# Optimization experiments

Measured on AMD Instinct MI355X. Metric: run time of the kernel, lower is better.

The kernel has to match this reference:

```python
import jax, jax.numpy as jnp
import numpy as np
import math

DIM = 1024
MAX_DEPTH = 16
ROPE_BASE = 10000.0
NUM_ACTIVE = 2

def setup_inputs() -> dict:
    key = jax.random.key(0)
    ks = jax.random.split(key, 6)
    bsz, seq, dim, E, hidden = 4, 1024, DIM, 8, 4 * DIM
    bound = 1.0 / math.sqrt(dim)
    return {
        "x": jax.random.normal(ks[0], (bsz, seq, dim), jnp.float32),
        "router_w": jax.random.normal(ks[1], (dim, dim), jnp.float32) * 0.02,
        "expert_keys": jax.random.uniform(ks[2], (E, dim), jnp.float32, -bound, bound),
        "expert_bias": jnp.zeros((E,), jnp.float32),
        "fc_w": jax.random.normal(ks[3], (E, hidden, dim), jnp.float32) * 0.02,
        "proj_w": jax.random.normal(ks[4], (E, dim, hidden), jnp.float32) * 0.02,
        "depth_idx": 3,
    }

def _rope_row(depth_idx, rev_idx, dtype):
    half = DIM // 2
    inv_freq = 1.0 / (ROPE_BASE ** (jnp.arange(0, DIM, 2, dtype=jnp.float32) / DIM))  # [half]
    f = depth_idx * inv_freq
    r = rev_idx * inv_freq
    return (jnp.cos(f).astype(dtype), jnp.sin(f).astype(dtype),
            jnp.cos(r).astype(dtype), jnp.sin(r).astype(dtype))

def reference(x, router_w, expert_keys, expert_bias, fc_w, proj_w, depth_idx):
    bsz, seq, dim = x.shape
    N = bsz * seq
    flat_x = x.reshape(N, dim)
    # router + RMSNorm (no weight, eps = machine eps, matching F.rms_norm default)
    q = flat_x @ router_w.T
    eps = jnp.asarray(jnp.finfo(q.dtype).eps, q.dtype)
    q = q * jax.lax.rsqrt(jnp.mean(q * q, axis=-1, keepdims=True) + eps)
    # depth RoPE (forward freq on first half pairing, reverse freq on second half)
    half = dim // 2
    cos, sin, rcos, rsin = _rope_row(float(depth_idx), float(MAX_DEPTH - 1 - depth_idx), q.dtype)
    q1, q2 = q[..., :half], q[..., half:]
    q = jnp.concatenate((q1 * cos + q2 * sin, -q1 * rsin + q2 * rcos), axis=-1)
    # routing
    logits = (q @ expert_keys.T) / math.sqrt(dim)  # [N, E]
    gate_values = jax.nn.sigmoid(logits)
    biased = logits + expert_bias
    _, topk_idx = jax.lax.top_k(biased, NUM_ACTIVE)  # [N, k]
    topk_gates = jnp.take_along_axis(gate_values, topk_idx, axis=-1)
    topk_gates = topk_gates / jnp.clip(topk_gates.sum(-1, keepdims=True), 1e-9, None)
    gates = jnp.zeros_like(gate_values).at[jnp.arange(N)[:, None], topk_idx].set(topk_gates)
    # dense all-expert MLP: relu(x W_fc^T)^2 W_proj^T, then mask-and-sum
    h = jax.nn.relu(jnp.einsum('nd,ehd->neh', flat_x, fc_w))
    expert_out = jnp.einsum('neh,edh->ned', h * h, proj_w)  # [N, E, dim]
    y = jnp.einsum('ned,ne->nd', expert_out, gates)
    return y.reshape(bsz, seq, dim)
```

## Files before the change

### kernel.cpp

```cpp
#include <hip/hip_runtime.h>
#include <hip/hip_bf16.h>
#include <math.h>

#define N_TOK 4096
#define DIM_V 1024
#define NEXP  8
#define HID   4096
#define NSLOT 9216

typedef short  s16x8 __attribute__((ext_vector_type(8)));
typedef unsigned short u16x8 __attribute__((ext_vector_type(8)));
typedef float  f32x4 __attribute__((ext_vector_type(4)));

constexpr size_t OFF_XB   = 0;
constexpr size_t OFF_WB   = OFF_XB + 8388608;
constexpr size_t OFF_RK   = OFF_WB + 2097152;
constexpr size_t OFF_KPP  = OFF_RK + 65536;
constexpr size_t OFF_SSQ  = OFF_KPP + 65536;
constexpr size_t OFF_CNT  = OFF_SSQ + 16384;
constexpr size_t OFF_CUR  = OFF_CNT + 128;
constexpr size_t OFF_TOK  = OFF_CUR + 128;
constexpr size_t OFF_GSL  = OFF_TOK + 36864;
constexpr size_t ZERO_BEG = OFF_KPP;
constexpr size_t ZERO_END = OFF_GSL + 36864;
constexpr size_t OFF_OFFP = ZERO_END;
constexpr size_t OFF_IDX2 = OFF_OFFP + 128;
constexpr size_t OFF_G2   = OFF_IDX2 + 32768;
constexpr size_t OFF_INV  = OFF_G2 + 32768;
constexpr size_t SMALL_END = OFF_INV + 32768;

constexpr size_t A_OFF_FCB = SMALL_END;
constexpr size_t A_OFF_PO  = A_OFF_FCB;
constexpr size_t A_OFF_PJB = A_OFF_FCB + 67108864;
constexpr size_t A_OFF_H2  = A_OFF_PJB + 67108864;
constexpr size_t WS_FULL   = A_OFF_H2 + 75497472;

__device__ inline unsigned short f2bf(float f) {
  __hip_bfloat16 h = __float2bfloat16(f);
  return __builtin_bit_cast(unsigned short, h);
}

__device__ __forceinline__ void gload16(const void* g, void* l) {
  __builtin_amdgcn_global_load_lds(
      (const __attribute__((address_space(1))) unsigned int*)g,
      (__attribute__((address_space(3))) unsigned int*)l, 16, 0, 0);
}

__global__ __launch_bounds__(256) void k_cvt_all(
    const float* __restrict__ x, const float* __restrict__ rw,
    const float* __restrict__ fw, const float* __restrict__ pw,
    unsigned short* __restrict__ xb, unsigned short* __restrict__ wb,
    unsigned short* __restrict__ fcb, unsigned short* __restrict__ pjb) {
  constexpr int NX = (N_TOK * DIM_V) / 4;
  constexpr int NW = (DIM_V * DIM_V) / 4;
  constexpr int NF = (NEXP * HID * DIM_V) / 4;
  const int cb[5] = {0, NX, NX + NW, NX + NW + NF, NX + NW + 2 * NF};
  const float* sp[4] = {x, rw, fw, pw};
  unsigned short* dp[4] = {xb, wb, fcb, pjb};
  const int total = cb[4];
  const int per = (total + (int)gridDim.x - 1) / (int)gridDim.x;
  const int beg = (int)blockIdx.x * per;
  const int end = (beg + per < total) ? beg + per : total;
#pragma unroll
  for (int r = 0; r < 4; ++r) {
    int rb = beg > cb[r] ? beg : cb[r];
    int re = end < cb[r + 1] ? end : cb[r + 1];
    const float4* s = (const float4*)sp[r];
    unsigned short* d = dp[r];
    for (int i = rb + (int)threadIdx.x; i < re; i += 256) {
      int j = i - cb[r];
      float4 v = s[j];
      ushort4 o = { f2bf(v.x), f2bf(v.y), f2bf(v.z), f2bf(v.w) };
      *(ushort4*)(d + (size_t)j * 4) = o;
    }
  }
}

__global__ void k_ropekeys(const float* __restrict__ keys, const int* __restrict__ depth,
                           double* __restrict__ rk) {
  int i = threadIdx.x;
  if (i >= 512) return;
  int dep = depth[0];
  double p = pow(10000.0, (double)i / 512.0);
  float invf = 1.0f / (float)p;
  float ff = (float)dep * invf;
  float rr = (float)(15 - dep) * invf;
  float cf  = (float)cos((double)ff);
  float sf  = (float)sin((double)ff);
  float rcf = (float)cos((double)rr);
  float rsf = (float)sin((double)rr);
  for (int e = 0; e < NEXP; ++e) {
    double k1 = (double)keys[e * DIM_V + i];
    double k2 = (double)keys[e * DIM_V + 512 + i];
    rk[e * DIM_V + i]       = (double)cf  * k1 - (double)rsf * k2;
    rk[e * DIM_V + 512 + i] = (double)sf  * k1 + (double)rcf * k2;
  }
}

__global__ __launch_bounds__(256) void k_colsum(const float* __restrict__ W,
                                                const double* __restrict__ rk,
                                                double* __restrict__ kpp) {
  int j  = blockIdx.x * 256 + threadIdx.x;
  int d0 = blockIdx.y * 64;
  double acc[NEXP] = {};
  for (int dd = 0; dd < 64; ++dd) {
    int d = d0 + dd;
    double w = (double)W[(size_t)d * DIM_V + j];
#pragma unroll
    for (int e = 0; e < NEXP; ++e) acc[e] += w * rk[e * DIM_V + d];
  }
  for (int e = 0; e < NEXP; ++e) atomicAdd(&kpp[e * DIM_V + j], acc[e]);
}

__global__ __launch_bounds__(256) void k_gate(const float* __restrict__ x,
                                              const double* __restrict__ kpp,
                                              const float* __restrict__ sumsq,
                                              const float* __restrict__ bias,
                                              int* __restrict__ idx2, float* __restrict__ gates2,
                                              int* __restrict__ counts) {
  int wave = (blockIdx.x * 256 + threadIdx.x) >> 6;
  int lane = threadIdx.x & 63;
  if (wave >= N_TOK) return;
  const float4* xr = (const float4*)(x + (size_t)wave * DIM_V);
  double a[NEXP] = {};
#pragma unroll
  for (int j = 0; j < 4; ++j) {
    int c = lane + 64 * j;
    float4 v = xr[c];
#pragma unroll
    for (int e = 0; e < NEXP; ++e) {
      const double* kp = kpp + (size_t)e * DIM_V + c * 4;
      a[e] += (double)v.x * kp[0] + (double)v.y * kp[1] +
              (double)v.z * kp[2] + (double)v.w * kp[3];
    }
  }
#pragma unroll
  for (int e = 0; e < NEXP; ++e)
    for (int d = 1; d < 64; d <<= 1) a[e] += __shfl_xor(a[e], d, 64);
  if (lane == 0) {
    float s = rsqrtf(sumsq[wave] * (1.0f / 1024.0f) + 1.1920928955078125e-7f);
    float z[NEXP], b[NEXP];
#pragma unroll
    for (int e = 0; e < NEXP; ++e) {
      z[e] = (float)(a[e] * (double)s * (1.0 / 32.0));
      b[e] = z[e] + bias[e];
    }
    int i1 = 0;
    for (int e = 1; e < NEXP; ++e) if (b[e] > b[i1]) i1 = e;
    int i2 = -1;
    for (int e = 0; e < NEXP; ++e) if (e != i1 && (i2 < 0 || b[e] > b[i2])) i2 = e;
    float g1 = 1.f / (1.f + expf(-z[i1]));
    float g2 = 1.f / (1.f + expf(-z[i2]));
    float sm = fmaxf(g1 + g2, 1e-9f);
    idx2[wave * 2] = i1; idx2[wave * 2 + 1] = i2;
    gates2[wave * 2] = g1 / sm; gates2[wave * 2 + 1] = g2 / sm;
    atomicAdd(&counts[i1], 1); atomicAdd(&counts[i2], 1);
  }
}

__global__ void k_scatter(const int* __restrict__ idx2, const float* __restrict__ gates2,
                          const int* __restrict__ counts, int* __restrict__ cursor,
                          int* __restrict__ tok, float* __restrict__ gsl,
                          int* __restrict__ inv, int* __restrict__ offp_out) {
  int off[NEXP + 1];
  off[0] = 0;
  for (int e = 0; e < NEXP; ++e) off[e + 1] = off[e] + ((counts[e] + 127) & ~127);
  int n = blockIdx.x * 256 + threadIdx.x;
  if (blockIdx.x == 0 && threadIdx.x == 0)
    for (int e = 0; e <= NEXP; ++e) offp_out[e] = off[e];
  if (n >= N_TOK) return;
  for (int r = 0; r < 2; ++r) {
    int e = idx2[n * 2 + r];
    int pos = atomicAdd(&cursor[e], 1);
    int slot = off[e] + pos;
    tok[slot] = n; gsl[slot] = gates2[n * 2 + r]; inv[n * 2 + r] = slot;
  }
}

__global__ __launch_bounds__(512) void k_fc256(
    const unsigned short* __restrict__ xb,
    const unsigned short* __restrict__ fcb,
    const int* __restrict__ offp, const int* __restrict__ tok,
    unsigned short* __restrict__ h2) {
  constexpr int KD = DIM_V;
  constexpr int NT = KD / 64;
  const int G = gridDim.x, q = G >> 3;
  const int idp = ((int)blockIdx.x & 7) * q + ((int)blockIdx.x >> 3);
  const int bx = idp >> 4;
  const int n0 = (idp & 15) * 256;
  int c = 0, e = 0, m0 = -1;
  for (e = 0; e < NEXP; ++e) {
    int nb = (offp[e + 1] - offp[e] + 255) >> 8;
    if (bx < c + nb) { m0 = offp[e] + (bx - c) * 256; break; }
    c += nb;
  }
  if (m0 < 0) return;
  const int segend = offp[e + 1];
  const unsigned short* Bp = fcb + ((size_t)e * HID + n0) * KD;

  __shared__ alignas(16) char smem[131072];
  const int tid = threadIdx.x, wid = tid >> 6, lane = tid & 63;
  const int wr = (wid >> 2) * 128, wcc = (wid & 3) * 64;
  const int swc8 = ((tid & 7) ^ ((tid >> 3) & 7)) * 8;
  const int frow = lane & 15, fsl = lane >> 4, fkey = lane & 7;

  int arow[4];
#pragma unroll
  for (int p = 0; p < 4; ++p) {
    int rr = m0 + p * 64 + (tid >> 3);
    arow[p] = tok[rr < NSLOT ? rr : NSLOT - 1];
  }

  auto stage = [&](int k0s, unsigned db) {
#pragma unroll
    for (int p = 0; p < 4; ++p)
      gload16(xb + (size_t)arow[p] * KD + k0s + swc8,
              smem + db + p * 8192 + wid * 1024);
#pragma unroll
    for (int p = 0; p < 4; ++p)
      gload16(Bp + (size_t)(p * 64 + (tid >> 3)) * KD + k0s + swc8,
              smem + db + 32768 + p * 8192 + wid * 1024);
  };

  f32x4 acc[8][4] = {};
  stage(0, 0);
  for (int t = 0; t < NT; ++t) {
    int tn = t + 1; if (tn == NT) tn = 0;
    stage(tn * 64, (unsigned)((t + 1) & 1) * 65536u);
    asm volatile("s_waitcnt vmcnt(8)" ::: "memory");
    __builtin_amdgcn_s_barrier();
    __builtin_amdgcn_sched_barrier(0);
    const unsigned Ab = (unsigned)(t & 1) * 65536u, Bb = Ab + 32768u;
#pragma unroll
    for (int kk2 = 0; kk2 < 2; ++kk2) {
      const unsigned so = (unsigned)(((fsl + kk2 * 4) ^ fkey) << 4);
      s16x8 af[8], bfr[4];
#pragma unroll
      for (int m = 0; m < 8; ++m)
        af[m] = *(const s16x8*)(smem + Ab + (unsigned)(wr + m * 16 + frow) * 128 + so);
#pragma unroll
      for (int n = 0; n < 4; ++n)
        bfr[n] = *(const s16x8*)(smem + Bb + (unsigned)(wcc + n * 16 + frow) * 128 + so);
      __builtin_amdgcn_s_setprio(1);
#pragma unroll
      for (int m = 0; m < 8; ++m)
#pragma unroll
        for (int n = 0; n < 4; ++n)
          acc[m][n] = __builtin_amdgcn_mfma_f32_16x16x32_bf16(af[m], bfr[n], acc[m][n], 0, 0, 0);
      __builtin_amdgcn_s_setprio(0);
    }
    __builtin_amdgcn_sched_barrier(0);
    __builtin_amdgcn_s_barrier();
  }
#pragma unroll
  for (int m = 0; m < 8; ++m)
#pragma unroll
    for (int j = 0; j < 4; ++j) {
      const int grow = m0 + wr + m * 16 + (lane >> 4) * 4 + j;
      if (grow < segend) {
#pragma unroll
        for (int n = 0; n < 4; ++n) {
          float v = acc[m][n][j];
          v = v > 0.f ? v * v : 0.f;
          h2[(size_t)grow * HID + n0 + wcc + n * 16 + (lane & 15)] = f2bf(v);
        }
      }
    }
}

__global__ __launch_bounds__(512) void k_proj256(
    const unsigned short* __restrict__ h2,
    const unsigned short* __restrict__ pjb,
    const int* __restrict__ offp, const float* __restrict__ gsl,
    float* __restrict__ po) {
  constexpr int KD = HID;
  constexpr int NT = KD / 64;
  const int G = gridDim.x, q = G >> 3;
  const int idp = ((int)blockIdx.x & 7) * q + ((int)blockIdx.x >> 3);
  const int bx = idp >> 4;
  const int n0 = (idp & 15) * 64;
  int c = 0, e = 0, m0 = -1;
  for (e = 0; e < NEXP; ++e) {
    int nb = (offp[e + 1] - offp[e] + 255) >> 8;
    if (bx < c + nb) { m0 = offp[e] + (bx - c) * 256; break; }
    c += nb;
  }
  if (m0 < 0) return;
  const int segend = offp[e + 1];
  const unsigned short* Bp = pjb + ((size_t)e * DIM_V + n0) * KD;

  __shared__ alignas(16) char smem[81920];
  const int tid = threadIdx.x, wid = tid >> 6, lane = tid & 63;
  const int wr = (wid >> 1) * 64, wc = (wid & 1) * 32;
  const int swc8 = ((tid & 7) ^ ((tid >> 3) & 7)) * 8;
  const int frow = lane & 15, fsl = lane >> 4, fkey = lane & 7;

  int arow[4];
#pragma unroll
  for (int p = 0; p < 4; ++p) {
    int rr = m0 + p * 64 + (tid >> 3);
    arow[p] = rr < NSLOT ? rr : NSLOT - 1;
  }

  auto stage = [&](int k0s, unsigned db) {
#pragma unroll
    for (int p = 0; p < 4; ++p)
      gload16(h2 + (size_t)arow[p] * KD + k0s + swc8,
              smem + db + p * 8192 + wid * 1024);
    gload16(Bp + (size_t)(tid >> 3) * KD + k0s + swc8,
            smem + db + 32768 + wid * 1024);
  };

  f32x4 acc[4][2] = {};
  stage(0, 0);
  for (int t = 0; t < NT; ++t) {
    int tn = t + 1; if (tn == NT) tn = 0;
    stage(tn * 64, (unsigned)((t + 1) & 1) * 40960u);
    asm volatile("s_waitcnt vmcnt(5)" ::: "memory");
    __builtin_amdgcn_s_barrier();
    __builtin_amdgcn_sched_barrier(0);
    const unsigned Ab = (unsigned)(t & 1) * 40960u, Bb = Ab + 32768u;
#pragma unroll
    for (int kk2 = 0; kk2 < 2; ++kk2) {
      const unsigned so = (unsigned)(((fsl + kk2 * 4) ^ fkey) << 4);
      s16x8 af[4], bfr[2];
#pragma unroll
      for (int m = 0; m < 4; ++m)
        af[m] = *(const s16x8*)(smem + Ab + (unsigned)(wr + m * 16 + frow) * 128 + so);
#pragma unroll
      for (int n = 0; n < 2; ++n)
        bfr[n] = *(const s16x8*)(smem + Bb + (unsigned)(wc + n * 16 + frow) * 128 + so);
      __builtin_amdgcn_s_setprio(1);
#pragma unroll
      for (int m = 0; m < 4; ++m)
#pragma unroll
        for (int n = 0; n < 2; ++n)
          acc[m][n] = __builtin_amdgcn_mfma_f32_16x16x32_bf16(af[m], bfr[n], acc[m][n], 0, 0, 0);
      __builtin_amdgcn_s_setprio(0);
    }
    __builtin_amdgcn_sched_barrier(0);
    __builtin_amdgcn_s_barrier();
  }
#pragma unroll
  for (int m = 0; m < 4; ++m)
#pragma unroll
    for (int j = 0; j < 4; ++j) {
      const int grow = m0 + wr + m * 16 + (lane >> 4) * 4 + j;
      if (grow < segend) {
        const float g = gsl[grow];
#pragma unroll
        for (int n = 0; n < 2; ++n)
          po[(size_t)grow * DIM_V + n0 + wc + n * 16 + (lane & 15)] = acc[m][n][j] * g;
      }
    }
}

__global__ __launch_bounds__(256) void k_qt(
    const unsigned short* __restrict__ Aptr,
    const unsigned short* __restrict__ Wptr,
    float* __restrict__ sumsq) {
  constexpr int KD = DIM_V;
  constexpr int GNB = DIM_V / 128;
  constexpr int NT  = KD / 64;
  const int G = gridDim.x, q = G >> 3;
  const int idp = ((int)blockIdx.x & 7) * q + ((int)blockIdx.x >> 3);
  const int n0 = (idp % GNB) * 128, m0 = (idp / GNB) * 128;
  const unsigned short* Bp = Wptr + (size_t)n0 * KD;

  __shared__ alignas(16) char smem[65536];
  const int tid = threadIdx.x, wid = tid >> 6, lane = tid & 63;
  const int wr = (wid >> 1) * 64, wc = (wid & 1) * 64;
  const int rql  = tid >> 3;
  const int swc8 = ((tid & 7) ^ ((tid >> 3) & 7)) * 8;
  const int frow = lane & 15, fsl = lane >> 4, fkey = lane & 7;

  auto stage = [&](int k0s, unsigned db) {
#pragma unroll
    for (int p = 0; p < 4; ++p)
      gload16(Aptr + (size_t)(m0 + p * 32 + rql) * KD + k0s + swc8,
              smem + db + p * 4096 + wid * 1024);
#pragma unroll
    for (int p = 0; p < 4; ++p)
      gload16(Bp + (size_t)(p * 32 + rql) * KD + k0s + swc8,
              smem + db + 16384 + p * 4096 + wid * 1024);
  };

  f32x4 acc[4][4] = {};
  stage(0, 0);
#pragma unroll 2
  for (int t = 0; t < NT; ++t) {
    int tn = t + 1; if (tn == NT) tn = 0;
    stage(tn * 64, (unsigned)((t + 1) & 1) * 32768u);
    asm volatile("s_waitcnt vmcnt(8)" ::: "memory");
    __builtin_amdgcn_s_barrier();
    __builtin_amdgcn_sched_barrier(0);
    const unsigned Ab = (unsigned)(t & 1) * 32768u, Bb = Ab + 16384u;
    s16x8 af[2][4], bfr[2][4];
#pragma unroll
    for (int kk2 = 0; kk2 < 2; ++kk2) {
      const unsigned so = (unsigned)(((fsl + kk2 * 4) ^ fkey) << 4);
#pragma unroll
      for (int m = 0; m < 4; ++m)
        af[kk2][m] = *(const s16x8*)(smem + Ab + (unsigned)(wr + m * 16 + frow) * 128 + so);
#pragma unroll
      for (int n = 0; n < 4; ++n)
        bfr[kk2][n] = *(const s16x8*)(smem + Bb + (unsigned)(wc + n * 16 + frow) * 128 + so);
    }
    __builtin_amdgcn_s_setprio(1);
#pragma unroll
    for (int kk2 = 0; kk2 < 2; ++kk2)
#pragma unroll
      for (int m = 0; m < 4; ++m)
#pragma unroll
        for (int n = 0; n < 4; ++n)
          acc[m][n] = __builtin_amdgcn_mfma_f32_16x16x32_bf16(af[kk2][m], bfr[kk2][n],
                                                              acc[m][n], 0, 0, 0);
    __builtin_amdgcn_s_setprio(0);
    __builtin_amdgcn_sched_barrier(0);
    __builtin_amdgcn_s_barrier();
  }

#pragma unroll
  for (int m = 0; m < 4; ++m)
#pragma unroll
    for (int j = 0; j < 4; ++j) {
      const int grow = m0 + wr + m * 16 + (lane >> 4) * 4 + j;
      float s = 0.f;
#pragma unroll
      for (int n = 0; n < 4; ++n) { float v = acc[m][n][j]; s += v * v; }
      s += __shfl_xor(s, 1, 64); s += __shfl_xor(s, 2, 64);
      s += __shfl_xor(s, 4, 64); s += __shfl_xor(s, 8, 64);
      if ((lane & 15) == 0) atomicAdd(&sumsq[grow], s);
    }
}

__global__ void k_combine(const float* __restrict__ po, const int* __restrict__ inv,
                          float* __restrict__ y) {
  const int total = N_TOK * (DIM_V / 4);
  for (int i = blockIdx.x * blockDim.x + threadIdx.x; i < total;
       i += gridDim.x * blockDim.x) {
    int n = i >> 8, c = i & 255;
    int s1 = inv[n * 2], s2 = inv[n * 2 + 1];
    float4 a = ((const float4*)(po + (size_t)s1 * DIM_V))[c];
    float4 b = ((const float4*)(po + (size_t)s2 * DIM_V))[c];
    float4 o; o.x = a.x + b.x; o.y = a.y + b.y; o.z = a.z + b.z; o.w = a.w + b.w;
    ((float4*)(y + (size_t)n * DIM_V))[c] = o;
  }
}

extern "C" void kernel_launch(void* const* d_in, const int* in_sizes, int n_in,
                              void* d_out, int out_size, void* d_ws, size_t ws_size,
                              hipStream_t stream) {
  if (ws_size < WS_FULL) return;
  const float* x      = (const float*)d_in[0];
  const float* rw     = (const float*)d_in[1];
  const float* keys   = (const float*)d_in[2];
  const float* bias   = (const float*)d_in[3];
  const float* fc_w   = (const float*)d_in[4];
  const float* proj_w = (const float*)d_in[5];
  const int*   depth  = (const int*)d_in[6];
  char* ws = (char*)d_ws;
  unsigned short* xb  = (unsigned short*)(ws + OFF_XB);
  unsigned short* wb  = (unsigned short*)(ws + OFF_WB);
  double* rk    = (double*)(ws + OFF_RK);
  double* kpp   = (double*)(ws + OFF_KPP);
  float*  ssq   = (float*)(ws + OFF_SSQ);
  int*    cnt   = (int*)(ws + OFF_CNT);
  int*    cur   = (int*)(ws + OFF_CUR);
  int*    tok   = (int*)(ws + OFF_TOK);
  float*  gsl   = (float*)(ws + OFF_GSL);
  int*    offp  = (int*)(ws + OFF_OFFP);
  int*    idx2  = (int*)(ws + OFF_IDX2);
  float*  g2    = (float*)(ws + OFF_G2);
  int*    inv   = (int*)(ws + OFF_INV);
  unsigned short* fcb = (unsigned short*)(ws + A_OFF_FCB);
  unsigned short* pjb = (unsigned short*)(ws + A_OFF_PJB);
  unsigned short* h2  = (unsigned short*)(ws + A_OFF_H2);
  float*  po    = (float*)(ws + A_OFF_PO);
  float*  y     = (float*)d_out;

  hipMemsetAsync(ws + ZERO_BEG, 0, ZERO_END - ZERO_BEG, stream);
  k_cvt_all<<<2048, 256, 0, stream>>>(x, rw, fc_w, proj_w, xb, wb, fcb, pjb);
  k_ropekeys<<<1, 512, 0, stream>>>(keys, depth, rk);
  k_colsum<<<dim3(4, 16), 256, 0, stream>>>(rw, rk, kpp);
  k_qt<<<dim3(32 * 8), 256, 0, stream>>>(xb, wb, ssq);
  k_gate<<<1024, 256, 0, stream>>>(x, kpp, ssq, bias, idx2, g2, cnt);
  k_scatter<<<16, 256, 0, stream>>>(idx2, g2, cnt, cur, tok, gsl, inv, offp);
  k_fc256<<<dim3(44 * 16), 512, 0, stream>>>(xb, fcb, offp, tok, h2);
  k_proj256<<<dim3(44 * 16), 512, 0, stream>>>(h2, pjb, offp, gsl, po);
  k_combine<<<2048, 256, 0, stream>>>(po, inv, y);
}
```

Before: 483.1 us.

## Triple-buffer LDS staging in GEMM kernels and widen bf16 conversion stores

```diff
diff --git a/kernel.cpp b/kernel.cpp
--- a/kernel.cpp
+++ b/kernel.cpp
@@ -51,9 +51,9 @@
     const float* __restrict__ fw, const float* __restrict__ pw,
     unsigned short* __restrict__ xb, unsigned short* __restrict__ wb,
     unsigned short* __restrict__ fcb, unsigned short* __restrict__ pjb) {
-  constexpr int NX = (N_TOK * DIM_V) / 4;
-  constexpr int NW = (DIM_V * DIM_V) / 4;
-  constexpr int NF = (NEXP * HID * DIM_V) / 4;
+  constexpr int NX = (N_TOK * DIM_V) / 16;
+  constexpr int NW = (DIM_V * DIM_V) / 16;
+  constexpr int NF = (NEXP * HID * DIM_V) / 16;
   const int cb[5] = {0, NX, NX + NW, NX + NW + NF, NX + NW + 2 * NF};
   const float* sp[4] = {x, rw, fw, pw};
   unsigned short* dp[4] = {xb, wb, fcb, pjb};
@@ -68,10 +68,17 @@
     const float4* s = (const float4*)sp[r];
     unsigned short* d = dp[r];
     for (int i = rb + (int)threadIdx.x; i < re; i += 256) {
-      int j = i - cb[r];
-      float4 v = s[j];
-      ushort4 o = { f2bf(v.x), f2bf(v.y), f2bf(v.z), f2bf(v.w) };
-      *(ushort4*)(d + (size_t)j * 4) = o;
+      size_t j = (size_t)(i - cb[r]);
+      float4 v0 = s[j * 4 + 0];
+      float4 v1 = s[j * 4 + 1];
+      float4 v2 = s[j * 4 + 2];
+      float4 v3 = s[j * 4 + 3];
+      u16x8 o0 = { f2bf(v0.x), f2bf(v0.y), f2bf(v0.z), f2bf(v0.w),
+                   f2bf(v1.x), f2bf(v1.y), f2bf(v1.z), f2bf(v1.w) };
+      u16x8 o1 = { f2bf(v2.x), f2bf(v2.y), f2bf(v2.z), f2bf(v2.w),
+                   f2bf(v3.x), f2bf(v3.y), f2bf(v3.z), f2bf(v3.w) };
+      *(u16x8*)(d + j * 16)     = o0;
+      *(u16x8*)(d + j * 16 + 8) = o1;
     }
   }
 }
@@ -289,7 +296,7 @@
   const int segend = offp[e + 1];
   const unsigned short* Bp = pjb + ((size_t)e * DIM_V + n0) * KD;
 
-  __shared__ alignas(16) char smem[81920];
+  __shared__ alignas(16) char smem[122880];
   const int tid = threadIdx.x, wid = tid >> 6, lane = tid & 63;
   const int wr = (wid >> 1) * 64, wc = (wid & 1) * 32;
   const int swc8 = ((tid & 7) ^ ((tid >> 3) & 7)) * 8;
@@ -312,14 +319,17 @@
   };
 
   f32x4 acc[4][2] = {};
-  stage(0, 0);
+  stage(0, 0u);
+  stage(64, 40960u);
+  int ci = 0;
   for (int t = 0; t < NT; ++t) {
-    int tn = t + 1; if (tn == NT) tn = 0;
-    stage(tn * 64, (unsigned)((t + 1) & 1) * 40960u);
-    asm volatile("s_waitcnt vmcnt(5)" ::: "memory");
+    int si = ci + 2; if (si >= 3) si -= 3;
+    int tn2 = t + 2; if (tn2 >= NT) tn2 -= NT;
+    stage(tn2 * 64, (unsigned)si * 40960u);
+    asm volatile("s_waitcnt vmcnt(10)" ::: "memory");
     __builtin_amdgcn_s_barrier();
     __builtin_amdgcn_sched_barrier(0);
-    const unsigned Ab = (unsigned)(t & 1) * 40960u, Bb = Ab + 32768u;
+    const unsigned Ab = (unsigned)ci * 40960u, Bb = Ab + 32768u;
 #pragma unroll
     for (int kk2 = 0; kk2 < 2; ++kk2) {
       const unsigned so = (unsigned)(((fsl + kk2 * 4) ^ fkey) << 4);
@@ -340,6 +350,7 @@
     }
     __builtin_amdgcn_sched_barrier(0);
     __builtin_amdgcn_s_barrier();
+    ci = ci + 1; if (ci == 3) ci = 0;
   }
 #pragma unroll
   for (int m = 0; m < 4; ++m)
@@ -367,7 +378,7 @@
   const int n0 = (idp % GNB) * 128, m0 = (idp / GNB) * 128;
   const unsigned short* Bp = Wptr + (size_t)n0 * KD;
 
-  __shared__ alignas(16) char smem[65536];
+  __shared__ alignas(16) char smem[98304];
   const int tid = threadIdx.x, wid = tid >> 6, lane = tid & 63;
   const int wr = (wid >> 1) * 64, wc = (wid & 1) * 64;
   const int rql  = tid >> 3;
@@ -386,15 +397,17 @@
   };
 
   f32x4 acc[4][4] = {};
-  stage(0, 0);
-#pragma unroll 2
+  stage(0, 0u);
+  stage(64, 32768u);
+  int ci = 0;
   for (int t = 0; t < NT; ++t) {
-    int tn = t + 1; if (tn == NT) tn = 0;
-    stage(tn * 64, (unsigned)((t + 1) & 1) * 32768u);
-    asm volatile("s_waitcnt vmcnt(8)" ::: "memory");
+    int si = ci + 2; if (si >= 3) si -= 3;
+    int tn2 = t + 2; if (tn2 >= NT) tn2 -= NT;
+    stage(tn2 * 64, (unsigned)si * 32768u);
+    asm volatile("s_waitcnt vmcnt(16)" ::: "memory");
     __builtin_amdgcn_s_barrier();
     __builtin_amdgcn_sched_barrier(0);
-    const unsigned Ab = (unsigned)(t & 1) * 32768u, Bb = Ab + 16384u;
+    const unsigned Ab = (unsigned)ci * 32768u, Bb = Ab + 16384u;
     s16x8 af[2][4], bfr[2][4];
 #pragma unroll
     for (int kk2 = 0; kk2 < 2; ++kk2) {
@@ -418,6 +431,7 @@
     __builtin_amdgcn_s_setprio(0);
     __builtin_amdgcn_sched_barrier(0);
     __builtin_amdgcn_s_barrier();
+    ci = ci + 1; if (ci == 3) ci = 0;
   }
 
 #pragma unroll
```

Measured after the change: 506.8 us. 1.05x slower.
